# Performance work log

Measured on AMD Instinct MI355X. Metric: run time of the kernel, lower is better.

The kernel has to match this reference:

```python
import jax, jax.numpy as jnp
import numpy as np
import math

D_MODEL = 512
N_HEADS = 8
HEAD_DIM = D_MODEL // N_HEADS


def setup_inputs() -> dict:
    key = jax.random.key(0)
    k1, k2, k3 = jax.random.split(key, 3)
    B, T = 2, 4096
    x = jax.random.normal(k1, (B, T, D_MODEL), dtype=jnp.float32)
    # nn.Linear weights: stored as [out, in], applied as x @ W.T
    W_QKV = jax.random.normal(k2, (3 * D_MODEL, D_MODEL), dtype=jnp.float32) * (1.0 / math.sqrt(D_MODEL))
    W_O = jax.random.normal(k3, (D_MODEL, D_MODEL), dtype=jnp.float32) * (1.0 / math.sqrt(D_MODEL))
    return {"x": x, "W_QKV": W_QKV, "W_O": W_O}


def reference(x, W_QKV, W_O):
    B, T, C = x.shape
    qkv = (x @ W_QKV.T).reshape(B, T, 3, N_HEADS, HEAD_DIM)
    q, k, v = qkv[:, :, 0], qkv[:, :, 1], qkv[:, :, 2]  # [B,T,H,D]
    # scores: [B,H,T,T]
    scale = math.sqrt(HEAD_DIM)
    attn = jnp.einsum('bqhd,bkhd->bhqk', q, k) / scale
    causal_mask = jnp.triu(jnp.ones((T, T), dtype=bool), k=1)
    attn = jnp.where(causal_mask, -jnp.inf, attn)
    attn = jax.nn.softmax(attn, axis=-1)
    out = jnp.einsum('bhqk,bkhd->bqhd', attn, v).reshape(B, T, C)
    return out @ W_O.T
```

## Files before the change

### kernel.cpp

```cpp
#include <hip/hip_runtime.h>
#include <hip/hip_bf16.h>

typedef __bf16 bf16_t;
typedef __bf16 bf16x8 __attribute__((ext_vector_type(8)));
typedef __bf16 bf16x4 __attribute__((ext_vector_type(4)));
typedef float  floatx4 __attribute__((ext_vector_type(4)));

static __device__ __forceinline__ floatx4 mfma16(bf16x8 a, bf16x8 b, floatx4 c) {
  return __builtin_amdgcn_mfma_f32_16x16x32_bf16(a, b, c, 0, 0, 0);
}

typedef __attribute__((address_space(3))) void lds_vp;
typedef __attribute__((address_space(1))) void glb_vp;
#define GLDS16(g, l) \
  __builtin_amdgcn_global_load_lds((glb_vp*)(g), (lds_vp*)(l), 16, 0, 0)

__global__ void cvt_all_kernel(const float* __restrict__ x,
                               const float* __restrict__ wqkv,
                               const float* __restrict__ wo,
                               bf16_t* __restrict__ xb,
                               bf16_t* __restrict__ wqkvb,
                               bf16_t* __restrict__ wob) {
  int i = blockIdx.x * blockDim.x + threadIdx.x;
  const float4* src; bf16x4* dst; int off;
  if (i < 1048576)      { src = (const float4*)x;    dst = (bf16x4*)xb;    off = i; }
  else if (i < 1245184) { src = (const float4*)wqkv; dst = (bf16x4*)wqkvb; off = i - 1048576; }
  else                  { src = (const float4*)wo;   dst = (bf16x4*)wob;   off = i - 1245184; }
  float4 v = src[off];
  bf16x4 o;
  o[0] = (bf16_t)v.x; o[1] = (bf16_t)v.y; o[2] = (bf16_t)v.z; o[3] = (bf16_t)v.w;
  dst[off] = o;
}

__global__ __launch_bounds__(256) void gemm_qkv(
    const bf16_t* __restrict__ A, const bf16_t* __restrict__ B,
    bf16_t* __restrict__ Qo, bf16_t* __restrict__ Ko, bf16_t* __restrict__ Vto)
{
  __shared__ __align__(16) bf16_t As[2][128 * 64];
  __shared__ __align__(16) bf16_t Bs[2][128 * 64];
  const int tid  = threadIdx.x;
  const int lane = tid & 63;
  const int w    = tid >> 6;
  const int quad = lane >> 4;
  const int l15  = lane & 15;
  const int l7   = lane & 7;
  const int wm   = w & 1;
  const int wn   = w >> 1;
  const int K    = 512;

  floatx4 acc[4][4];
  #pragma unroll
  for (int i = 0; i < 4; ++i)
    #pragma unroll
    for (int j = 0; j < 4; ++j)
      acc[i][j] = (floatx4){0.f, 0.f, 0.f, 0.f};

  const bf16_t* Ab = A + (size_t)blockIdx.x * 128 * K;
  const bf16_t* Bb = B + (size_t)blockIdx.y * 128 * K;

  auto stage = [&](int buf, int k0) {
    #pragma unroll
    for (int i = 0; i < 4; ++i) {
      int c = tid + 256 * i;
      int row = c >> 3, colc = c & 7;
      int gofs = ((colc ^ (row & 7)) << 3);
      GLDS16(&Ab[(size_t)row * K + k0 + gofs], &As[buf][c * 8]);
      GLDS16(&Bb[(size_t)row * K + k0 + gofs], &Bs[buf][c * 8]);
    }
  };

  stage(0, 0);
  for (int it = 0; it < 8; ++it) {
    const int cur = it & 1;
    __syncthreads();
    if (it + 1 < 8) stage(cur ^ 1, (it + 1) << 6);
    #pragma unroll
    for (int ks = 0; ks < 2; ++ks) {
      bf16x8 af[4], bfr[4];
      #pragma unroll
      for (int t = 0; t < 4; ++t) {
        af[t]  = *(const bf16x8*)&As[cur][(wm * 64 + t * 16 + l15) * 64 +
                                         (((ks * 4 + quad) ^ l7) << 3)];
        bfr[t] = *(const bf16x8*)&Bs[cur][(wn * 64 + t * 16 + l15) * 64 +
                                         (((ks * 4 + quad) ^ l7) << 3)];
      }
      #pragma unroll
      for (int mt = 0; mt < 4; ++mt)
        #pragma unroll
        for (int nt = 0; nt < 4; ++nt)
          acc[mt][nt] = mfma16(af[mt], bfr[nt], acc[mt][nt]);
    }
  }

  if (blockIdx.y < 8) {
    #pragma unroll
    for (int mt = 0; mt < 4; ++mt) {
      #pragma unroll
      for (int nt = 0; nt < 4; ++nt) {
        #pragma unroll
        for (int r = 0; r < 4; ++r) {
          int m = blockIdx.x * 128 + wm * 64 + mt * 16 + quad * 4 + r;
          int n = blockIdx.y * 128 + wn * 64 + nt * 16 + l15;
          float v = acc[mt][nt][r];
          int b = m >> 12, t = m & 4095;
          int h = (n >> 6) & 7, d = n & 63;
          size_t bh = (size_t)(b * 8 + h);
          if (n < 512)
            Qo[bh * 262144 + (size_t)t * 64 + d] = (bf16_t)(v * 0.18033688f);
          else
            Ko[bh * 262144 + (size_t)t * 64 + d] = (bf16_t)v;
        }
      }
    }
  } else {
    __syncthreads();
    bf16_t* L = &As[0][0];
    #pragma unroll
    for (int mt = 0; mt < 4; ++mt)
      #pragma unroll
      for (int nt = 0; nt < 4; ++nt) {
        int n_l = wn * 64 + nt * 16 + l15;
        int mc  = wm * 8 + mt * 2 + (quad >> 1);
        bf16x4 v4;
        #pragma unroll
        for (int r = 0; r < 4; ++r) v4[r] = (bf16_t)acc[mt][nt][r];
        *(bf16x4*)&L[n_l * 128 + ((mc ^ (n_l & 15)) << 3) + (quad & 1) * 4] = v4;
      }
    __syncthreads();
    const int t0 = (blockIdx.x & 31) * 128;
    const int b  = blockIdx.x >> 5;
    #pragma unroll
    for (int i = 0; i < 8; ++i) {
      int c = tid + 256 * i;
      int n_l = c >> 4, tc = c & 15;
      int h = ((blockIdx.y - 8) << 1) | (n_l >> 6);
      int d = n_l & 63;
      size_t bh = (size_t)(b * 8 + h);
      int base0 = (tc >> 2) * 32 + (tc & 3) * 4;
      bf16x4 lo = *(const bf16x4*)&L[n_l * 128 +
                     (((base0 >> 3) ^ (n_l & 15)) << 3) + (base0 & 7)];
      bf16x4 hi = *(const bf16x4*)&L[n_l * 128 +
                     ((((base0 + 16) >> 3) ^ (n_l & 15)) << 3) + (base0 & 7)];
      bf16x8 o;
      #pragma unroll
      for (int e = 0; e < 4; ++e) { o[e] = lo[e]; o[e + 4] = hi[e]; }
      *(bf16x8*)&Vto[bh * 262144 + (size_t)d * 4096 + t0 + tc * 8] = o;
    }
  }
}

__global__ __launch_bounds__(256) void gemm_out(
    const bf16_t* __restrict__ A, const bf16_t* __restrict__ B,
    float* __restrict__ Cf)
{
  __shared__ __align__(16) bf16_t As[2][64 * 64];
  __shared__ __align__(16) bf16_t Bs[2][128 * 64];
  const int tid  = threadIdx.x;
  const int lane = tid & 63;
  const int w    = tid >> 6;
  const int quad = lane >> 4;
  const int l15  = lane & 15;
  const int l7   = lane & 7;

  floatx4 acc[4][2];
  #pragma unroll
  for (int i = 0; i < 4; ++i)
    #pragma unroll
    for (int j = 0; j < 2; ++j)
      acc[i][j] = (floatx4){0.f, 0.f, 0.f, 0.f};

  const bf16_t* Ab = A + (size_t)blockIdx.x * 64 * 512;
  const bf16_t* Bb = B + (size_t)blockIdx.y * 128 * 512;

  auto stage = [&](int buf, int k0) {
    #pragma unroll
    for (int i = 0; i < 2; ++i) {
      int c = tid + 256 * i;
      int row = c >> 3, colc = c & 7;
      GLDS16(&Ab[(size_t)row * 512 + k0 + ((colc ^ (row & 7)) << 3)],
             &As[buf][c * 8]);
    }
    #pragma unroll
    for (int i = 0; i < 4; ++i) {
      int c = tid + 256 * i;
      int row = c >> 3, colc = c & 7;
      GLDS16(&Bb[(size_t)row * 512 + k0 + ((colc ^ (row & 7)) << 3)],
             &Bs[buf][c * 8]);
    }
  };

  stage(0, 0);
  for (int it = 0; it < 8; ++it) {
    const int cur = it & 1;
    __syncthreads();
    if (it + 1 < 8) stage(cur ^ 1, (it + 1) << 6);
    #pragma unroll
    for (int ks = 0; ks < 2; ++ks) {
      bf16x8 af[4], bfr[2];
      #pragma unroll
      for (int t = 0; t < 4; ++t)
        af[t]  = *(const bf16x8*)&As[cur][(t * 16 + l15) * 64 +
                                         (((ks * 4 + quad) ^ l7) << 3)];
      #pragma unroll
      for (int t = 0; t < 2; ++t)
        bfr[t] = *(const bf16x8*)&Bs[cur][(w * 32 + t * 16 + l15) * 64 +
                                         (((ks * 4 + quad) ^ l7) << 3)];
      #pragma unroll
      for (int mt = 0; mt < 4; ++mt)
        #pragma unroll
        for (int nt = 0; nt < 2; ++nt)
          acc[mt][nt] = mfma16(af[mt], bfr[nt], acc[mt][nt]);
    }
  }

  #pragma unroll
  for (int mt = 0; mt < 4; ++mt)
    #pragma unroll
    for (int nt = 0; nt < 2; ++nt)
      #pragma unroll
      for (int r = 0; r < 4; ++r) {
        int m = blockIdx.x * 64 + mt * 16 + quad * 4 + r;
        int n = blockIdx.y * 128 + w * 32 + nt * 16 + l15;
        Cf[(size_t)m * 512 + n] = acc[mt][nt][r];
      }
}

__global__ __launch_bounds__(512, 2) void attn_kernel(
    const bf16_t* __restrict__ Qg, const bf16_t* __restrict__ Kgl,
    const bf16_t* __restrict__ Vtg, bf16_t* __restrict__ Og)
{
  __shared__ __align__(16) bf16_t Ks[2][128 * 64];
  __shared__ __align__(16) bf16_t Vts[2][64 * 128];

  const int tid  = threadIdx.x;
  const int lane = tid & 63;
  const int w    = tid >> 6;
  const int grp2 = w >> 1;
  const int tileB = grp2 >> 1;
  const int half  = grp2 & 1;
  const int ws2   = w & 1;
  const int quad = lane >> 4;
  const int l15  = lane & 15;

  const int id = blockIdx.x;
  const int k8 = id & 7;
  const int j  = id >> 3;
  const int bh = 2 * k8 + (j & 1);
  const int x  = j >> 1;
  const int qtA = 31 - x, qtB = x;
  const int qt_g = tileB ? qtB : qtA;
  const size_t bh_off = (size_t)bh * 262144;
  const int b = bh >> 3, h = bh & 7;

  const int gq0 = qt_g * 128 + half * 64 + ws2 * 32 + l15;
  bf16x8 aqk0[2], aqk1[2];
  #pragma unroll
  for (int qb = 0; qb < 2; ++qb) {
    const bf16_t* Qp = Qg + bh_off + (size_t)(gq0 + qb * 16) * 64;
    aqk0[qb] = *(const bf16x8*)&Qp[quad * 8];
    aqk1[qb] = *(const bf16x8*)&Qp[32 + quad * 8];
  }
  bf16x8 ones;
  #pragma unroll
  for (int i = 0; i < 8; ++i) ones[i] = (bf16_t)1.0f;

  floatx4 acc_o[2][4], acc_l[2];
  #pragma unroll
  for (int qb = 0; qb < 2; ++qb) {
    #pragma unroll
    for (int dt = 0; dt < 4; ++dt) acc_o[qb][dt] = (floatx4){0.f, 0.f, 0.f, 0.f};
    acc_l[qb] = (floatx4){0.f, 0.f, 0.f, 0.f};
  }

  auto stage = [&](int buf, int kt) {
    const bf16_t* Kp = Kgl + bh_off + (size_t)kt * 8192;
    const bf16_t* Vp = Vtg + bh_off + (size_t)kt * 128;
    #pragma unroll
    for (int i = 0; i < 2; ++i) {
      int c = tid + 512 * i;
      int row = c >> 3, colc = c & 7;
      GLDS16(&Kp[row * 64 + ((colc ^ (row & 7)) << 3)], &Ks[buf][c * 8]);
    }
    #pragma unroll
    for (int i = 0; i < 2; ++i) {
      int c = tid + 512 * i;
      int row = c >> 4, colc = c & 15;
      GLDS16(&Vp[(size_t)row * 4096 + ((colc ^ (row & 15)) << 3)], &Vts[buf][c * 8]);
    }
  };

  stage(0, 0);
  const int nkt = qtA + 1;
  const floatx4 z4 = (floatx4){0.f, 0.f, 0.f, 0.f};
  for (int kt = 0; kt < nkt; ++kt) {
    const int cur = kt & 1;
    __syncthreads();
    if (kt + 1 < nkt) stage(cur ^ 1, kt + 1);

    if (kt <= qt_g) {
      floatx4 s[2][8];
      #pragma unroll
      for (int nt = 0; nt < 8; ++nt) {
        bf16x8 bk0 = *(const bf16x8*)&Ks[cur][(nt * 16 + l15) * 64 +
                                             ((quad ^ (l15 & 7)) << 3)];
        s[0][nt] = mfma16(bk0, aqk0[0], z4);
        s[1][nt] = mfma16(bk0, aqk0[1], z4);
      }
      #pragma unroll
      for (int nt = 0; nt < 8; ++nt) {
        bf16x8 bk1 = *(const bf16x8*)&Ks[cur][(nt * 16 + l15) * 64 +
                                             (((4 + quad) ^ (l15 & 7)) << 3)];
        s[0][nt] = mfma16(bk1, aqk1[0], s[0][nt]);
        s[1][nt] = mfma16(bk1, aqk1[1], s[1][nt]);
      }

      if (kt == qt_g) {
        #pragma unroll
        for (int qb = 0; qb < 2; ++qb)
          #pragma unroll
          for (int nt = 0; nt < 8; ++nt)
            #pragma unroll
            for (int r = 0; r < 4; ++r)
              if (kt * 128 + nt * 16 + quad * 4 + r > gq0 + qb * 16)
                s[qb][nt][r] = -3.0e38f;
      }
      #pragma unroll
      for (int qb = 0; qb < 2; ++qb)
        #pragma unroll
        for (int nt = 0; nt < 8; ++nt)
          #pragma unroll
          for (int r = 0; r < 4; ++r)
            s[qb][nt][r] = __builtin_amdgcn_exp2f(s[qb][nt][r]);

      #pragma unroll
      for (int kc = 0; kc < 4; ++kc) {
        bf16x8 pb[2];
        #pragma unroll
        for (int qb = 0; qb < 2; ++qb)
          #pragma unroll
          for (int r = 0; r < 4; ++r) {
            pb[qb][r]     = (bf16_t)s[qb][kc * 2][r];
            pb[qb][r + 4] = (bf16_t)s[qb][kc * 2 + 1][r];
          }
        acc_l[0] = mfma16(ones, pb[0], acc_l[0]);
        acc_l[1] = mfma16(ones, pb[1], acc_l[1]);
        #pragma unroll
        for (int dt = 0; dt < 4; ++dt) {
          int row = dt * 16 + l15;
          bf16x8 av = *(const bf16x8*)&Vts[cur][row * 128 +
                                               (((kc * 4 + quad) ^ l15) << 3)];
          acc_o[0][dt] = mfma16(av, pb[0], acc_o[0][dt]);
          acc_o[1][dt] = mfma16(av, pb[1], acc_o[1][dt]);
        }
      }
    }
  }

  __syncthreads();
  bf16_t* Ot = &Ks[0][grp2 * 4096];
  #pragma unroll
  for (int qb = 0; qb < 2; ++qb) {
    const float rl = 1.0f / acc_l[qb][0];
    const int t_own = ws2 * 32 + qb * 16 + l15;
    #pragma unroll
    for (int dt = 0; dt < 4; ++dt) {
      bf16x4 o4;
      #pragma unroll
      for (int r = 0; r < 4; ++r) o4[r] = (bf16_t)(acc_o[qb][dt][r] * rl);
      *(bf16x4*)&Ot[t_own * 64 +
                    (((dt * 2 + (quad >> 1)) ^ (t_own & 7)) << 3) + (quad & 1) * 4] = o4;
    }
  }
  __syncthreads();
  const int gtid = tid & 127;
  #pragma unroll
  for (int i = 0; i < 4; ++i) {
    int cc = gtid + 128 * i;
    int t = cc >> 3, c = cc & 7;
    bf16x8 o8 = *(const bf16x8*)&Ot[t * 64 + ((c ^ (t & 7)) << 3)];
    int trow = qt_g * 128 + half * 64 + t;
    *(bf16x8*)&Og[((size_t)b * 4096 + trow) * 512 + h * 64 + c * 8] = o8;
  }
}

extern "C" void kernel_launch(void* const* d_in, const int* in_sizes, int n_in,
                              void* d_out, int out_size, void* d_ws, size_t ws_size,
                              hipStream_t stream) {
  const float* x    = (const float*)d_in[0];
  const float* wqkv = (const float*)d_in[1];
  const float* wo   = (const float*)d_in[2];
  float* out = (float*)d_out;

  char* ws = (char*)d_ws;
  bf16_t* xb    = (bf16_t*)(ws);
  bf16_t* wqkvb = (bf16_t*)(ws + 8388608);
  bf16_t* wob   = (bf16_t*)(ws + 9961472);
  bf16_t* Qb    = (bf16_t*)(ws + 10485760);
  bf16_t* Kb    = (bf16_t*)(ws + 18874368);
  bf16_t* Vtb   = (bf16_t*)(ws + 27262976);
  bf16_t* Ob    = xb;

  cvt_all_kernel<<<5120, 256, 0, stream>>>(x, wqkv, wo, xb, wqkvb, wob);

  gemm_qkv<<<dim3(64, 12), 256, 0, stream>>>(xb, wqkvb, Qb, Kb, Vtb);
  attn_kernel<<<dim3(256), 512, 0, stream>>>(Qb, Kb, Vtb, Ob);
  gemm_out<<<dim3(128, 4), 256, 0, stream>>>(Ob, wob, out);
}
```

Before: 153.0 us.

## Split attention key tiles across wave pairs with 64-query register blocking and LDS reduction

Measured after the change: 147.4 us. 3.7% less time.

```diff
diff --git a/kernel.cpp b/kernel.cpp
--- a/kernel.cpp
+++ b/kernel.cpp
@@ -229,16 +229,16 @@
     const bf16_t* __restrict__ Qg, const bf16_t* __restrict__ Kgl,
     const bf16_t* __restrict__ Vtg, bf16_t* __restrict__ Og)
 {
-  __shared__ __align__(16) bf16_t Ks[2][128 * 64];
-  __shared__ __align__(16) bf16_t Vts[2][64 * 128];
+  __shared__ __align__(16) bf16_t smem[49664];
+  bf16_t* KsB  = smem;
+  bf16_t* VtsB = smem + 16384;
 
   const int tid  = threadIdx.x;
   const int lane = tid & 63;
   const int w    = tid >> 6;
-  const int grp2 = w >> 1;
-  const int tileB = grp2 >> 1;
-  const int half  = grp2 & 1;
-  const int ws2   = w & 1;
+  const int tile = w >> 2;
+  const int qh   = (w >> 1) & 1;
+  const int kh   = w & 1;
   const int quad = lane >> 4;
   const int l15  = lane & 15;
 
@@ -248,25 +248,26 @@
   const int bh = 2 * k8 + (j & 1);
   const int x  = j >> 1;
   const int qtA = 31 - x, qtB = x;
-  const int qt_g = tileB ? qtB : qtA;
+  const int qt_g = tile ? qtB : qtA;
+  const int qt2  = qt_g * 2 + qh;
   const size_t bh_off = (size_t)bh * 262144;
   const int b = bh >> 3, h = bh & 7;
 
-  const int gq0 = qt_g * 128 + half * 64 + ws2 * 32 + l15;
-  bf16x8 aqk0[2], aqk1[2];
-  #pragma unroll
-  for (int qb = 0; qb < 2; ++qb) {
-    const bf16_t* Qp = Qg + bh_off + (size_t)(gq0 + qb * 16) * 64;
-    aqk0[qb] = *(const bf16x8*)&Qp[quad * 8];
-    aqk1[qb] = *(const bf16x8*)&Qp[32 + quad * 8];
+  const int qbase = qt_g * 128 + qh * 64;
+  bf16x8 aq0[4], aq1[4];
+  #pragma unroll
+  for (int qb = 0; qb < 4; ++qb) {
+    const bf16_t* Qp = Qg + bh_off + (size_t)(qbase + qb * 16 + l15) * 64;
+    aq0[qb] = *(const bf16x8*)&Qp[quad * 8];
+    aq1[qb] = *(const bf16x8*)&Qp[32 + quad * 8];
   }
   bf16x8 ones;
   #pragma unroll
   for (int i = 0; i < 8; ++i) ones[i] = (bf16_t)1.0f;
 
-  floatx4 acc_o[2][4], acc_l[2];
-  #pragma unroll
-  for (int qb = 0; qb < 2; ++qb) {
+  floatx4 acc_o[4][4], acc_l[4];
+  #pragma unroll
+  for (int qb = 0; qb < 4; ++qb) {
     #pragma unroll
     for (int dt = 0; dt < 4; ++dt) acc_o[qb][dt] = (floatx4){0.f, 0.f, 0.f, 0.f};
     acc_l[qb] = (floatx4){0.f, 0.f, 0.f, 0.f};
@@ -279,13 +280,14 @@
     for (int i = 0; i < 2; ++i) {
       int c = tid + 512 * i;
       int row = c >> 3, colc = c & 7;
-      GLDS16(&Kp[row * 64 + ((colc ^ (row & 7)) << 3)], &Ks[buf][c * 8]);
+      GLDS16(&Kp[row * 64 + ((colc ^ (row & 7)) << 3)], &KsB[buf * 8192 + c * 8]);
     }
     #pragma unroll
     for (int i = 0; i < 2; ++i) {
       int c = tid + 512 * i;
       int row = c >> 4, colc = c & 15;
-      GLDS16(&Vp[(size_t)row * 4096 + ((colc ^ (row & 15)) << 3)], &Vts[buf][c * 8]);
+      GLDS16(&Vp[(size_t)row * 4096 + ((colc ^ (row & 15)) << 3)],
+             &VtsB[buf * 8192 + c * 8]);
     }
   };
 
@@ -297,89 +299,121 @@
     __syncthreads();
     if (kt + 1 < nkt) stage(cur ^ 1, kt + 1);
 
-    if (kt <= qt_g) {
-      floatx4 s[2][8];
-      #pragma unroll
-      for (int nt = 0; nt < 8; ++nt) {
-        bf16x8 bk0 = *(const bf16x8*)&Ks[cur][(nt * 16 + l15) * 64 +
-                                             ((quad ^ (l15 & 7)) << 3)];
-        s[0][nt] = mfma16(bk0, aqk0[0], z4);
-        s[1][nt] = mfma16(bk0, aqk0[1], z4);
-      }
-      #pragma unroll
-      for (int nt = 0; nt < 8; ++nt) {
-        bf16x8 bk1 = *(const bf16x8*)&Ks[cur][(nt * 16 + l15) * 64 +
-                                             (((4 + quad) ^ (l15 & 7)) << 3)];
-        s[0][nt] = mfma16(bk1, aqk1[0], s[0][nt]);
-        s[1][nt] = mfma16(bk1, aqk1[1], s[1][nt]);
-      }
-
-      if (kt == qt_g) {
-        #pragma unroll
-        for (int qb = 0; qb < 2; ++qb)
+    if (2 * kt + kh <= qt2) {
+      const bf16_t* Kc = &KsB[cur * 8192 + kh * 64 * 64];
+      const bf16_t* Vc = &VtsB[cur * 8192];
+      floatx4 s[4][4];
+      #pragma unroll
+      for (int nt = 0; nt < 4; ++nt) {
+        bf16x8 bk0 = *(const bf16x8*)&Kc[(nt * 16 + l15) * 64 +
+                                         ((quad ^ (l15 & 7)) << 3)];
+        s[0][nt] = mfma16(bk0, aq0[0], z4);
+        s[1][nt] = mfma16(bk0, aq0[1], z4);
+        s[2][nt] = mfma16(bk0, aq0[2], z4);
+        s[3][nt] = mfma16(bk0, aq0[3], z4);
+      }
+      #pragma unroll
+      for (int nt = 0; nt < 4; ++nt) {
+        bf16x8 bk1 = *(const bf16x8*)&Kc[(nt * 16 + l15) * 64 +
+                                         (((4 + quad) ^ (l15 & 7)) << 3)];
+        #pragma unroll
+        for (int qb = 0; qb < 4; ++qb)
+          s[qb][nt] = mfma16(bk1, aq1[qb], s[qb][nt]);
+      }
+
+      if (2 * kt + kh == qt2) {
+        #pragma unroll
+        for (int qb = 0; qb < 4; ++qb)
           #pragma unroll
-          for (int nt = 0; nt < 8; ++nt)
+          for (int nt = 0; nt < 4; ++nt)
             #pragma unroll
             for (int r = 0; r < 4; ++r)
-              if (kt * 128 + nt * 16 + quad * 4 + r > gq0 + qb * 16)
+              if (nt * 16 + quad * 4 + r > qb * 16 + l15)
                 s[qb][nt][r] = -3.0e38f;
       }
       #pragma unroll
-      for (int qb = 0; qb < 2; ++qb)
-        #pragma unroll
-        for (int nt = 0; nt < 8; ++nt)
+      for (int qb = 0; qb < 4; ++qb)
+        #pragma unroll
+        for (int nt = 0; nt < 4; ++nt)
           #pragma unroll
           for (int r = 0; r < 4; ++r)
             s[qb][nt][r] = __builtin_amdgcn_exp2f(s[qb][nt][r]);
 
       #pragma unroll
-      for (int kc = 0; kc < 4; ++kc) {
-        bf16x8 pb[2];
-        #pragma unroll
-        for (int qb = 0; qb < 2; ++qb)
+      for (int kc = 0; kc < 2; ++kc) {
+        bf16x8 pb[4];
+        #pragma unroll
+        for (int qb = 0; qb < 4; ++qb)
           #pragma unroll
           for (int r = 0; r < 4; ++r) {
             pb[qb][r]     = (bf16_t)s[qb][kc * 2][r];
             pb[qb][r + 4] = (bf16_t)s[qb][kc * 2 + 1][r];
           }
-        acc_l[0] = mfma16(ones, pb[0], acc_l[0]);
-        acc_l[1] = mfma16(ones, pb[1], acc_l[1]);
+        #pragma unroll
+        for (int qb = 0; qb < 4; ++qb)
+          acc_l[qb] = mfma16(ones, pb[qb], acc_l[qb]);
         #pragma unroll
         for (int dt = 0; dt < 4; ++dt) {
-          int row = dt * 16 + l15;
-          bf16x8 av = *(const bf16x8*)&Vts[cur][row * 128 +
-                                               (((kc * 4 + quad) ^ l15) << 3)];
-          acc_o[0][dt] = mfma16(av, pb[0], acc_o[0][dt]);
-          acc_o[1][dt] = mfma16(av, pb[1], acc_o[1][dt]);
+          bf16x8 av = *(const bf16x8*)&Vc[(dt * 16 + l15) * 128 +
+                         ((((kh * 2 + kc) * 4 + quad) ^ l15) << 3)];
+          #pragma unroll
+          for (int qb = 0; qb < 4; ++qb)
+            acc_o[qb][dt] = mfma16(av, pb[qb], acc_o[qb][dt]);
         }
       }
     }
   }
 
   __syncthreads();
-  bf16_t* Ot = &Ks[0][grp2 * 4096];
-  #pragma unroll
-  for (int qb = 0; qb < 2; ++qb) {
-    const float rl = 1.0f / acc_l[qb][0];
-    const int t_own = ws2 * 32 + qb * 16 + l15;
-    #pragma unroll
-    for (int dt = 0; dt < 4; ++dt) {
-      bf16x4 o4;
-      #pragma unroll
-      for (int r = 0; r < 4; ++r) o4[r] = (bf16_t)(acc_o[qb][dt][r] * rl);
-      *(bf16x4*)&Ot[t_own * 64 +
-                    (((dt * 2 + (quad >> 1)) ^ (t_own & 7)) << 3) + (quad & 1) * 4] = o4;
+  float*  PART = (float*)smem;
+  bf16_t* OUT  = smem + 33280;
+  const int p = w >> 1;
+  float* P = PART + p * 4160;
+
+  if (kh == 1) {
+    #pragma unroll
+    for (int qb = 0; qb < 4; ++qb) {
+      #pragma unroll
+      for (int dt = 0; dt < 4; ++dt) {
+        int chunk = (dt * 4 + quad) ^ l15;
+        *(floatx4*)&P[(qb * 16 + l15) * 64 + chunk * 4] = acc_o[qb][dt];
+      }
+      if (quad == 0) P[4096 + qb * 16 + l15] = acc_l[qb][0];
     }
   }
   __syncthreads();
-  const int gtid = tid & 127;
-  #pragma unroll
-  for (int i = 0; i < 4; ++i) {
-    int cc = gtid + 128 * i;
-    int t = cc >> 3, c = cc & 7;
-    bf16x8 o8 = *(const bf16x8*)&Ot[t * 64 + ((c ^ (t & 7)) << 3)];
-    int trow = qt_g * 128 + half * 64 + t;
-    *(bf16x8*)&Og[((size_t)b * 4096 + trow) * 512 + h * 64 + c * 8] = o8;
+  if (kh == 0) {
+    bf16_t* Ot = OUT + p * 4096;
+    #pragma unroll
+    for (int qb = 0; qb < 4; ++qb) {
+      const int t_own = qb * 16 + l15;
+      float rl = 1.0f / (acc_l[qb][0] + P[4096 + t_own]);
+      #pragma unroll
+      for (int dt = 0; dt < 4; ++dt) {
+        int chunk = (dt * 4 + quad) ^ l15;
+        floatx4 pp = *(const floatx4*)&P[t_own * 64 + chunk * 4];
+        bf16x4 o4;
+        #pragma unroll
+        for (int r = 0; r < 4; ++r)
+          o4[r] = (bf16_t)((acc_o[qb][dt][r] + pp[r]) * rl);
+        *(bf16x4*)&Ot[t_own * 64 +
+                      (((dt * 2 + (quad >> 1)) ^ (t_own & 7)) << 3) +
+                      (quad & 1) * 4] = o4;
+      }
+    }
+  }
+  __syncthreads();
+  {
+    bf16_t* Ot = OUT + p * 4096;
+    const int gtid = ((w & 1) << 6) | lane;
+    #pragma unroll
+    for (int i = 0; i < 4; ++i) {
+      int cc = gtid + 128 * i;
+      int t = cc >> 3, c = cc & 7;
+      bf16x8 o8 = *(const bf16x8*)&Ot[t * 64 + ((c ^ (t & 7)) << 3)];
+      int trow = qbase + t;
+      *(bf16x8*)&Og[((size_t)b * 4096 + trow) * 512 + h * 64 + c * 8] = o8;
+    }
   }
 }
 
```
